# Optimization experiments

Hardware: AMD Instinct MI355X
Metric: run time of the kernel (lower is better)

The kernel has to match this reference:

```python
import jax, jax.numpy as jnp
import numpy as np

NTOKEN, NINP, NHID = 50257, 256, 256
B, T = 64, 2048
RES, FC1 = 10, NHID // 3
EPS = 1e-5

def lrelu(x, p=0.01):
    return jnp.maximum(x, x * p)

def setup_inputs() -> dict:
    key = jax.random.key(0)
    ks = jax.random.split(key, 12)
    s = 0.05
    inp = {
        "input": jax.random.randint(ks[0], (B, T), 0, NTOKEN),
        "hx": jnp.zeros((B, NHID), jnp.float32),
        "cx": jnp.zeros((B, NHID), jnp.float32),
        "seq_len": jax.random.randint(ks[1], (B,), 1, T + 1),  # lengths in [1, T]
        "emb_w": jax.random.uniform(ks[2], (NTOKEN, NINP), jnp.float32, -0.1, 0.1),
        "W_ih": jax.random.normal(ks[3], (4 * NHID, NINP), jnp.float32) * s,
        "W_hh": jax.random.normal(ks[4], (4 * NHID, NHID), jnp.float32) * s,
        "b_ih": jnp.zeros((4 * NHID,), jnp.float32),
        "b_hh": jnp.zeros((4 * NHID,), jnp.float32),
        "rfc1_w": jax.random.normal(ks[5], (RES, NHID), jnp.float32) * s,
        "rfc1_b": jnp.zeros((RES,), jnp.float32),
        "rbn_g": jnp.ones((RES,), jnp.float32),
        "rbn_b": jnp.zeros((RES,), jnp.float32),
        "rbn_rm": jnp.zeros((RES,), jnp.float32),
        "rbn_rv": jnp.ones((RES,), jnp.float32),
        "rfc2_w": jax.random.normal(ks[6], (NHID, RES), jnp.float32) * s,
        "rfc2_b": jnp.zeros((NHID,), jnp.float32),
        "fc1_w": jax.random.normal(ks[7], (FC1, NHID), jnp.float32) * s,
        "fc1_b": jnp.zeros((FC1,), jnp.float32),
        "bn1_g": jnp.ones((FC1,), jnp.float32),
        "bn1_b": jnp.zeros((FC1,), jnp.float32),
        "bn1_rm": jnp.zeros((FC1,), jnp.float32),
        "bn1_rv": jnp.ones((FC1,), jnp.float32),
        "fc2_w": jax.random.normal(ks[8], (2, FC1), jnp.float32) * s,
        "fc2_b": jnp.zeros((2,), jnp.float32),
    }
    return inp

def reference(input, hx, cx, seq_len, emb_w, W_ih, W_hh, b_ih, b_hh,
              rfc1_w, rfc1_b, rbn_g, rbn_b, rbn_rm, rbn_rv, rfc2_w, rfc2_b,
              fc1_w, fc1_b, bn1_g, bn1_b, bn1_rm, bn1_rv, fc2_w, fc2_b):
    # eval mode: dropout = identity, noise = 0, BatchNorm uses running stats
    emb = emb_w[input.T]  # [T, B, ninp]
    # precompute input-side gates once (batched matmul) -> [T, B, 4*nhid]
    x_gates = jnp.einsum('tbi,gi->tbg', emb, W_ih) + b_ih + b_hh

    def step(carry, xg):
        h, c = carry
        gates = xg + h @ W_hh.T
        i, f, g, o = jnp.split(gates, 4, axis=-1)
        c = jax.nn.sigmoid(f) * c + jax.nn.sigmoid(i) * jnp.tanh(g)
        h = jax.nn.sigmoid(o) * jnp.tanh(c)
        return (h, c), h

    (hx_f, cx_f), outs = jax.lax.scan(step, (hx, cx), x_gates)  # outs: [T, B, nhid]

    # ragged mean pooling over first seq_len[b] steps
    mask = (jnp.arange(T)[:, None] < seq_len[None, :]).astype(outs.dtype)  # [T, B]
    feature = jnp.einsum('tbh,tb->bh', outs, mask) / seq_len[:, None].astype(outs.dtype)

    # ResNet block (eval)
    res = jax.nn.relu(feature) @ rfc1_w.T + rfc1_b
    res = jax.nn.relu(res)
    res = (res - rbn_rm) * jax.lax.rsqrt(rbn_rv + EPS) * rbn_g + rbn_b
    feature = feature + res @ rfc2_w.T + rfc2_b

    # classifier head
    fc = feature @ fc1_w.T + fc1_b
    fc = (fc - bn1_rm) * jax.lax.rsqrt(bn1_rv + EPS) * bn1_g + bn1_b
    fc = lrelu(fc)
    logits = fc @ fc2_w.T + fc2_b
    logp = jax.nn.log_softmax(logits, axis=-1)
    return (logp, hx_f, cx_f)
```

## Files before the change

### kernel.cpp

```cpp
#include <hip/hip_runtime.h>
#include <cstdint>


#define NTOKEN 50257
#define NINP 256
#define NHID 256
#define BB 64
#define TT 2048
#define NRES 10
#define NFC1 85
#define EPSV 1e-5f

typedef _Float16 f16;
typedef _Float16 f16x2 __attribute__((ext_vector_type(2)));
typedef _Float16 f16x8 __attribute__((ext_vector_type(8)));
typedef float f32x4 __attribute__((ext_vector_type(4)));

static __device__ __forceinline__ float sigm(float x) { return 1.0f / (1.0f + __expf(-x)); }
static __device__ __forceinline__ float tanh_(float x) {
  float ax = fabsf(x);
  float e = __expf(-2.0f * ax);
  float t = (1.0f - e) / (1.0f + e);
  return x < 0.0f ? -t : t;
}

static __device__ __forceinline__ float fdot2(f16x2 a, f16x2 b, float c) {
#if __has_builtin(__builtin_amdgcn_fdot2)
  return __builtin_amdgcn_fdot2(a, b, c, false);
#else
  return c + (float)a[0] * (float)b[0] + (float)a[1] * (float)b[1];
#endif
}

__global__ void k0_convert(const float* __restrict__ emb_w, const float* __restrict__ W_ih,
                           const float* __restrict__ b_ih, const float* __restrict__ b_hh,
                           f16* __restrict__ emb16, f16* __restrict__ wih16,
                           float* __restrict__ bias) {
  int64_t i = (int64_t)blockIdx.x * blockDim.x + threadIdx.x;
  if (i < (int64_t)NTOKEN * NINP) emb16[i] = (f16)emb_w[i];
  if (i < 4 * NHID * NINP) wih16[i] = (f16)W_ih[i];
  if (i < 4 * NHID) bias[i] = b_ih[i] + b_hh[i];
}

__global__ __launch_bounds__(256) void k1_gemm(const f16* __restrict__ emb16,
                                               const f16* __restrict__ wih16,
                                               const float* __restrict__ bias,
                                               f16* __restrict__ xgtab) {
  __shared__ __align__(16) f16 a_lds[64][40];
  __shared__ __align__(16) f16 b_lds[256][40];
  const int mt = blockIdx.x;
  const int nt0 = blockIdx.y * 256;
  const int tid = threadIdx.x;
  const int lane = tid & 63;
  const int w = tid >> 6;
  const int quad = lane >> 4;
  const int l16 = lane & 15;

  f32x4 acc[16];
#pragma unroll
  for (int i = 0; i < 16; i++) acc[i] = (f32x4){0.f, 0.f, 0.f, 0.f};

  const int ar = tid >> 2;
  int av = mt * 64 + ar;
  if (av > NTOKEN - 1) av = NTOKEN - 1;
  const int ac = (tid & 3) * 8;

  for (int kb = 0; kb < 256; kb += 32) {
    *(uint4*)&a_lds[ar][ac] = *(const uint4*)&emb16[av * 256 + kb + ac];
    {
      const uint4* bs = (const uint4*)&wih16[(nt0 + tid) * 256 + kb];
      uint4* bd = (uint4*)&b_lds[tid][0];
      bd[0] = bs[0]; bd[1] = bs[1]; bd[2] = bs[2]; bd[3] = bs[3];
    }
    __syncthreads();
    f16x8 af = *(const f16x8*)&a_lds[w * 16 + l16][quad * 8];
#pragma unroll
    for (int nt = 0; nt < 16; nt++) {
      f16x8 bf = *(const f16x8*)&b_lds[nt * 16 + l16][quad * 8];
      acc[nt] = __builtin_amdgcn_mfma_f32_16x16x32_f16(af, bf, acc[nt], 0, 0, 0);
    }
    __syncthreads();
  }
#pragma unroll
  for (int nt = 0; nt < 16; nt++) {
#pragma unroll
    for (int rg = 0; rg < 4; rg++) {
      int v = mt * 64 + w * 16 + quad * 4 + rg;
      if (v < NTOKEN) {
        int n = nt0 + nt * 16 + l16;
        xgtab[v * 1024 + n] = (f16)(acc[nt][rg] + bias[n]);
      }
    }
  }
}

#define RK 92
#define LK 36
__global__ __launch_bounds__(512, 2) void k2_rnn(
    const int* __restrict__ input, const float* __restrict__ hx0,
    const float* __restrict__ cx0, const int* __restrict__ seq_len,
    const float* __restrict__ Whh, const f16* __restrict__ xgtab,
    float* __restrict__ feat, float* __restrict__ out_hx, float* __restrict__ out_cx) {
  __shared__ uint2 lw2[LK * 512];
  __shared__ __align__(16) f16 hpak[NHID];
  __shared__ float fo_f[NHID];
  __shared__ float fo_o[NHID];

  const int b = blockIdx.x;
  const int tid = threadIdx.x;
  const int r0 = tid, r1 = tid + 512;

  unsigned int w0[RK], w1[RK];
#pragma unroll
  for (int m = 0; m < 128; m++) {
    float2 a = *(const float2*)&Whh[r0 * 256 + 2 * m];
    float2 d = *(const float2*)&Whh[r1 * 256 + 2 * m];
    f16x2 pa; pa[0] = (f16)a.x; pa[1] = (f16)a.y;
    f16x2 pd; pd[0] = (f16)d.x; pd[1] = (f16)d.y;
    unsigned int ua = __builtin_bit_cast(unsigned int, pa);
    unsigned int ud = __builtin_bit_cast(unsigned int, pd);
    if (m < RK) { w0[m] = ua; w1[m] = ud; }
    else { lw2[(m - RK) * 512 + tid] = make_uint2(ua, ud); }
  }

  float c = 0.0f, pool = 0.0f, hnew = 0.0f;
  if (tid < NHID) {
    hpak[tid] = (f16)hx0[b * NHID + tid];
    c = cx0[b * NHID + tid];
  }
  const int L = seq_len[b];
  __syncthreads();

  const int* tokp = input + b * TT;
  int tok_next = tokp[1];
  f16 xga, xgb;
  {
    int tok0 = tokp[0];
    xga = xgtab[tok0 * 1024 + r0];
    xgb = xgtab[tok0 * 1024 + r1];
  }

  for (int t = 0; t < TT; t++) {
    int tn = (t + 2 < TT) ? tokp[t + 2] : 0;
    f16 pfa = xgtab[tok_next * 1024 + r0];
    f16 pfb = xgtab[tok_next * 1024 + r1];

    float acc0 = (float)xga, acc1 = (float)xgb;
    const uint4* hp = (const uint4*)hpak;
#pragma unroll
    for (int mb = 0; mb < 32; mb++) {
      uint4 h4 = hp[mb];
#pragma unroll
      for (int j = 0; j < 4; j++) {
        const int m = mb * 4 + j;
        unsigned int hu = (j == 0) ? h4.x : (j == 1) ? h4.y : (j == 2) ? h4.z : h4.w;
        f16x2 hh = __builtin_bit_cast(f16x2, hu);
        f16x2 wa, wb;
        if (m < RK) {
          wa = __builtin_bit_cast(f16x2, w0[m]);
          wb = __builtin_bit_cast(f16x2, w1[m]);
        } else {
          uint2 ww = lw2[(m - RK) * 512 + tid];
          wa = __builtin_bit_cast(f16x2, ww.x);
          wb = __builtin_bit_cast(f16x2, ww.y);
        }
        acc0 = fdot2(wa, hh, acc0);
        acc1 = fdot2(wb, hh, acc1);
      }
    }

    if (tid >= NHID) {
      fo_f[tid - NHID] = sigm(acc0);
      fo_o[tid - NHID] = sigm(acc1);
    }
    __syncthreads();
    if (tid < NHID) {
      float ig = sigm(acc0);
      float gg = tanh_(acc1);
      c = fo_f[tid] * c + ig * gg;
      hnew = fo_o[tid] * tanh_(c);
      if (t < L) pool += hnew;
      hpak[tid] = (f16)hnew;
    }
    __syncthreads();
    xga = pfa; xgb = pfb; tok_next = tn;
  }

  if (tid < NHID) {
    feat[b * NHID + tid] = pool / (float)L;
    out_hx[b * NHID + tid] = hnew;
    out_cx[b * NHID + tid] = c;
  }
}

__global__ __launch_bounds__(256) void k3_head(const float* __restrict__ feat,
    const float* __restrict__ rfc1_w, const float* __restrict__ rfc1_b,
    const float* __restrict__ rbn_g, const float* __restrict__ rbn_b,
    const float* __restrict__ rbn_rm, const float* __restrict__ rbn_rv,
    const float* __restrict__ rfc2_w, const float* __restrict__ rfc2_b,
    const float* __restrict__ fc1_w, const float* __restrict__ fc1_b,
    const float* __restrict__ bn1_g, const float* __restrict__ bn1_b,
    const float* __restrict__ bn1_rm, const float* __restrict__ bn1_rv,
    const float* __restrict__ fc2_w, const float* __restrict__ fc2_b,
    float* __restrict__ logp) {
  __shared__ float f[256];
  __shared__ float f2[256];
  __shared__ float res[16];
  __shared__ float fcv[96];
  const int b = blockIdx.x, tid = threadIdx.x;
  const int wv = tid >> 6, lane = tid & 63;
  f[tid] = feat[b * 256 + tid];
  __syncthreads();
  for (int r = wv; r < NRES; r += 4) {
    float p = 0.f;
#pragma unroll
    for (int j0 = 0; j0 < 4; j0++) {
      int j = lane * 4 + j0;
      p += fmaxf(f[j], 0.f) * rfc1_w[r * 256 + j];
    }
    for (int off = 32; off > 0; off >>= 1) p += __shfl_down(p, off);
    if (lane == 0) {
      float x = p + rfc1_b[r];
      x = fmaxf(x, 0.f);
      x = (x - rbn_rm[r]) * rsqrtf(rbn_rv[r] + EPSV) * rbn_g[r] + rbn_b[r];
      res[r] = x;
    }
  }
  __syncthreads();
  {
    float s = rfc2_b[tid];
#pragma unroll
    for (int r = 0; r < NRES; r++) s += res[r] * rfc2_w[tid * NRES + r];
    f2[tid] = f[tid] + s;
  }
  __syncthreads();
  for (int o = wv; o < NFC1; o += 4) {
    float p = 0.f;
#pragma unroll
    for (int j0 = 0; j0 < 4; j0++) {
      int j = lane * 4 + j0;
      p += f2[j] * fc1_w[o * 256 + j];
    }
    for (int off = 32; off > 0; off >>= 1) p += __shfl_down(p, off);
    if (lane == 0) {
      float x = p + fc1_b[o];
      x = (x - bn1_rm[o]) * rsqrtf(bn1_rv[o] + EPSV) * bn1_g[o] + bn1_b[o];
      x = fmaxf(x, 0.01f * x);
      fcv[o] = x;
    }
  }
  __syncthreads();
  if (tid == 0) {
    float l0 = fc2_b[0], l1 = fc2_b[1];
    for (int o2 = 0; o2 < NFC1; o2++) {
      l0 += fcv[o2] * fc2_w[o2];
      l1 += fcv[o2] * fc2_w[NFC1 + o2];
    }
    float mx = fmaxf(l0, l1);
    float lse = mx + __logf(__expf(l0 - mx) + __expf(l1 - mx));
    logp[b * 2 + 0] = l0 - lse;
    logp[b * 2 + 1] = l1 - lse;
  }
}

extern "C" void kernel_launch(void* const* d_in, const int* in_sizes, int n_in,
                              void* d_out, int out_size, void* d_ws, size_t ws_size,
                              hipStream_t stream) {
  const int*   input  = (const int*)  d_in[0];
  const float* hx     = (const float*)d_in[1];
  const float* cx     = (const float*)d_in[2];
  const int*   seqlen = (const int*)  d_in[3];
  const float* emb_w  = (const float*)d_in[4];
  const float* W_ih   = (const float*)d_in[5];
  const float* W_hh   = (const float*)d_in[6];
  const float* b_ih   = (const float*)d_in[7];
  const float* b_hh   = (const float*)d_in[8];
  const float* rfc1_w = (const float*)d_in[9];
  const float* rfc1_b = (const float*)d_in[10];
  const float* rbn_g  = (const float*)d_in[11];
  const float* rbn_b  = (const float*)d_in[12];
  const float* rbn_rm = (const float*)d_in[13];
  const float* rbn_rv = (const float*)d_in[14];
  const float* rfc2_w = (const float*)d_in[15];
  const float* rfc2_b = (const float*)d_in[16];
  const float* fc1_w  = (const float*)d_in[17];
  const float* fc1_b  = (const float*)d_in[18];
  const float* bn1_g  = (const float*)d_in[19];
  const float* bn1_b  = (const float*)d_in[20];
  const float* bn1_rm = (const float*)d_in[21];
  const float* bn1_rv = (const float*)d_in[22];
  const float* fc2_w  = (const float*)d_in[23];
  const float* fc2_b  = (const float*)d_in[24];

  char* ws = (char*)d_ws;
  f16*   emb16 = (f16*)(ws);
  f16*   wih16 = (f16*)(ws + 25731584);
  float* bias  = (float*)(ws + 26255872);
  f16*   xgtab = (f16*)(ws + 26259968);
  float* feat  = (float*)(ws + 129186304);

  float* out = (float*)d_out;

  k0_convert<<<dim3(NTOKEN), 256, 0, stream>>>(emb_w, W_ih, b_ih, b_hh, emb16, wih16, bias);
  k1_gemm<<<dim3((NTOKEN + 63) / 64, 4), 256, 0, stream>>>(emb16, wih16, bias, xgtab);
  k2_rnn<<<dim3(BB), 512, 0, stream>>>(input, hx, cx, seqlen, W_hh, xgtab, feat,
                                       out + 128, out + 128 + BB * NHID);
  k3_head<<<dim3(BB), 256, 0, stream>>>(feat, rfc1_w, rfc1_b, rbn_g, rbn_b, rbn_rm, rbn_rv,
                                        rfc2_w, rfc2_b, fc1_w, fc1_b, bn1_g, bn1_b, bn1_rm,
                                        bn1_rv, fc2_w, fc2_b, out);
}
```

Baseline: 4.165 ms.

## Split LSTM recurrence across 1024 threads with K-partitioned weights and readlane broadcast

Restructures the recurrent kernel so each of 1024 threads owns one hidden unit's four gate rows over a quarter of the K dimension, holding most weights in registers and the rest in LDS. A separate pack kernel pre-converts W_hh to fp16 in this layout. Partial sums are reduced through LDS, and h values are broadcast with readlane instead of LDS vector reads. The aim is shorter per-step dot-product latency and fewer LDS reads on the serial critical path. In exchange it adds a cross-partition reduction and a one-block-per-batch launch at 1024 threads. The pack buffers reuse workspace memory that earlier kernels already consumed.

```diff
diff --git a/kernel.cpp b/kernel.cpp
--- a/kernel.cpp
+++ b/kernel.cpp
@@ -11,6 +11,9 @@
 #define NFC1 85
 #define EPSV 1e-5f
 
+#define QP 23
+#define LJ 9
+
 typedef _Float16 f16;
 typedef _Float16 f16x2 __attribute__((ext_vector_type(2)));
 typedef _Float16 f16x8 __attribute__((ext_vector_type(8)));
@@ -24,11 +27,12 @@
   return x < 0.0f ? -t : t;
 }
 
-static __device__ __forceinline__ float fdot2(f16x2 a, f16x2 b, float c) {
+static __device__ __forceinline__ float fdot2u(unsigned int a, unsigned int b, float c) {
 #if __has_builtin(__builtin_amdgcn_fdot2)
-  return __builtin_amdgcn_fdot2(a, b, c, false);
+  return __builtin_amdgcn_fdot2(__builtin_bit_cast(f16x2, a), __builtin_bit_cast(f16x2, b), c, false);
 #else
-  return c + (float)a[0] * (float)b[0] + (float)a[1] * (float)b[1];
+  f16x2 av = __builtin_bit_cast(f16x2, a), bv = __builtin_bit_cast(f16x2, b);
+  return c + (float)av[0] * (float)bv[0] + (float)av[1] * (float)bv[1];
 #endif
 }
 
@@ -94,102 +98,115 @@
   }
 }
 
-#define RK 92
-#define LK 36
-__global__ __launch_bounds__(512, 2) void k2_rnn(
+__global__ __launch_bounds__(128) void k0b_pack(const float* __restrict__ Whh,
+                                                unsigned int* __restrict__ wregq,
+                                                unsigned int* __restrict__ wldsq) {
+  const int R = blockIdx.x;
+  const int p = threadIdx.x;
+  float2 a = *(const float2*)&Whh[R * 256 + 2 * p];
+  f16x2 pk; pk[0] = (f16)a.x; pk[1] = (f16)a.y;
+  unsigned int uu = __builtin_bit_cast(unsigned int, pk);
+  int u = (R & 255) + 256 * (p >> 5);
+  int ri = R >> 8;
+  int pp = p & 31;
+  if (pp < QP) wregq[(pp * 1024 + u) * 4 + ri] = uu;
+  else         wldsq[((pp - QP) * 1024 + u) * 4 + ri] = uu;
+}
+
+__global__ __launch_bounds__(1024) void k2_rnn(
     const int* __restrict__ input, const float* __restrict__ hx0,
     const float* __restrict__ cx0, const int* __restrict__ seq_len,
-    const float* __restrict__ Whh, const f16* __restrict__ xgtab,
+    const uint4* __restrict__ wregq, const uint4* __restrict__ wldsq,
+    const f16* __restrict__ xgtab,
     float* __restrict__ feat, float* __restrict__ out_hx, float* __restrict__ out_cx) {
-  __shared__ uint2 lw2[LK * 512];
-  __shared__ __align__(16) f16 hpak[NHID];
-  __shared__ float fo_f[NHID];
-  __shared__ float fo_o[NHID];
+  __shared__ uint4 lw4[LJ * 1024];
+  __shared__ float part[3 * 256 * 4];
+  __shared__ f16 xbuf[1024];
+  __shared__ __align__(8) f16 hpak[NHID];
 
   const int b = blockIdx.x;
-  const int tid = threadIdx.x;
-  const int r0 = tid, r1 = tid + 512;
-
-  unsigned int w0[RK], w1[RK];
-#pragma unroll
-  for (int m = 0; m < 128; m++) {
-    float2 a = *(const float2*)&Whh[r0 * 256 + 2 * m];
-    float2 d = *(const float2*)&Whh[r1 * 256 + 2 * m];
-    f16x2 pa; pa[0] = (f16)a.x; pa[1] = (f16)a.y;
-    f16x2 pd; pd[0] = (f16)d.x; pd[1] = (f16)d.y;
-    unsigned int ua = __builtin_bit_cast(unsigned int, pa);
-    unsigned int ud = __builtin_bit_cast(unsigned int, pd);
-    if (m < RK) { w0[m] = ua; w1[m] = ud; }
-    else { lw2[(m - RK) * 512 + tid] = make_uint2(ua, ud); }
-  }
-
-  float c = 0.0f, pool = 0.0f, hnew = 0.0f;
-  if (tid < NHID) {
-    hpak[tid] = (f16)hx0[b * NHID + tid];
-    c = cx0[b * NHID + tid];
+  const int u = threadIdx.x;
+  const int lane = u & 63;
+  const int r = u & 255;
+  const int q = u >> 8;
+
+  uint4 w4[QP];
+#pragma unroll
+  for (int i = 0; i < QP; i++) w4[i] = wregq[i * 1024 + u];
+#pragma unroll
+  for (int j = 0; j < LJ; j++) lw4[j * 1024 + u] = wldsq[j * 1024 + u];
+
+  float c = 0.f, pool = 0.f, h = 0.f;
+  if (u < NHID) {
+    hpak[u] = (f16)hx0[b * NHID + u];
+    c = cx0[b * NHID + u];
   }
   const int L = seq_len[b];
-  __syncthreads();
-
   const int* tokp = input + b * TT;
-  int tok_next = tokp[1];
-  f16 xga, xgb;
   {
-    int tok0 = tokp[0];
-    xga = xgtab[tok0 * 1024 + r0];
-    xgb = xgtab[tok0 * 1024 + r1];
-  }
-
+    int tok0 = __builtin_amdgcn_readfirstlane(tokp[0]);
+    xbuf[u] = xgtab[(size_t)tok0 * 1024 + u];
+  }
+  __syncthreads();
+
+  const unsigned int* hpu = (const unsigned int*)hpak;
+  const int hoff = 32 * q + (lane & 31);
+  unsigned int hsel = hpu[hoff];
+
+  int toff = 0;
+#pragma unroll 1
   for (int t = 0; t < TT; t++) {
-    int tn = (t + 2 < TT) ? tokp[t + 2] : 0;
-    f16 pfa = xgtab[tok_next * 1024 + r0];
-    f16 pfb = xgtab[tok_next * 1024 + r1];
-
-    float acc0 = (float)xga, acc1 = (float)xgb;
-    const uint4* hp = (const uint4*)hpak;
-#pragma unroll
-    for (int mb = 0; mb < 32; mb++) {
-      uint4 h4 = hp[mb];
-#pragma unroll
-      for (int j = 0; j < 4; j++) {
-        const int m = mb * 4 + j;
-        unsigned int hu = (j == 0) ? h4.x : (j == 1) ? h4.y : (j == 2) ? h4.z : h4.w;
-        f16x2 hh = __builtin_bit_cast(f16x2, hu);
-        f16x2 wa, wb;
-        if (m < RK) {
-          wa = __builtin_bit_cast(f16x2, w0[m]);
-          wb = __builtin_bit_cast(f16x2, w1[m]);
-        } else {
-          uint2 ww = lw2[(m - RK) * 512 + tid];
-          wa = __builtin_bit_cast(f16x2, ww.x);
-          wb = __builtin_bit_cast(f16x2, ww.y);
-        }
-        acc0 = fdot2(wa, hh, acc0);
-        acc1 = fdot2(wb, hh, acc1);
-      }
-    }
-
-    if (tid >= NHID) {
-      fo_f[tid - NHID] = sigm(acc0);
-      fo_o[tid - NHID] = sigm(acc1);
+    int tk = __builtin_amdgcn_readfirstlane(tokp[(t + 1 < TT) ? t + 1 : TT - 1]);
+    f16 xn = xgtab[(size_t)tk * 1024 + u];
+
+    float a0 = 0.f, a1 = 0.f, a2 = 0.f, a3 = 0.f;
+#pragma unroll
+    for (int i = 0; i < QP; i++) {
+      unsigned int hs = (unsigned int)__builtin_amdgcn_readlane((int)hsel, i);
+      a0 = fdot2u(w4[i].x, hs, a0);
+      a1 = fdot2u(w4[i].y, hs, a1);
+      a2 = fdot2u(w4[i].z, hs, a2);
+      a3 = fdot2u(w4[i].w, hs, a3);
+    }
+#pragma unroll
+    for (int j = 0; j < LJ; j++) {
+      int je = j + toff; if (je >= LJ) je -= LJ;
+      uint4 w = lw4[je * 1024 + u];
+      unsigned int hs = (unsigned int)__builtin_amdgcn_readlane((int)hsel, QP + je);
+      a0 = fdot2u(w.x, hs, a0);
+      a1 = fdot2u(w.y, hs, a1);
+      a2 = fdot2u(w.z, hs, a2);
+      a3 = fdot2u(w.w, hs, a3);
+    }
+
+    if (q > 0) {
+      *(float4*)&part[((q - 1) * 256 + r) * 4] = make_float4(a0, a1, a2, a3);
     }
     __syncthreads();
-    if (tid < NHID) {
-      float ig = sigm(acc0);
-      float gg = tanh_(acc1);
-      c = fo_f[tid] * c + ig * gg;
-      hnew = fo_o[tid] * tanh_(c);
-      if (t < L) pool += hnew;
-      hpak[tid] = (f16)hnew;
+    if (q == 0) {
+      float4 p1 = *(const float4*)&part[(0 * 256 + r) * 4];
+      float4 p2 = *(const float4*)&part[(1 * 256 + r) * 4];
+      float4 p3 = *(const float4*)&part[(2 * 256 + r) * 4];
+      float gi = a0 + p1.x + p2.x + p3.x + (float)xbuf[r];
+      float gf = a1 + p1.y + p2.y + p3.y + (float)xbuf[NHID + r];
+      float gg = a2 + p1.z + p2.z + p3.z + (float)xbuf[2 * NHID + r];
+      float go = a3 + p1.w + p2.w + p3.w + (float)xbuf[3 * NHID + r];
+      float ig = sigm(gi), fg = sigm(gf), gt = tanh_(gg), og = sigm(go);
+      c = fg * c + ig * gt;
+      h = og * tanh_(c);
+      pool += (t < L) ? h : 0.f;
+      hpak[r] = (f16)h;
     }
     __syncthreads();
-    xga = pfa; xgb = pfb; tok_next = tn;
-  }
-
-  if (tid < NHID) {
-    feat[b * NHID + tid] = pool / (float)L;
-    out_hx[b * NHID + tid] = hnew;
-    out_cx[b * NHID + tid] = c;
+    hsel = hpu[hoff];
+    xbuf[u] = xn;
+    toff++; if (toff == LJ) toff = 0;
+  }
+
+  if (q == 0) {
+    feat[b * NHID + r] = pool / (float)L;
+    out_hx[b * NHID + r] = h;
+    out_cx[b * NHID + r] = c;
   }
 }
 
@@ -299,12 +316,17 @@
   f16*   xgtab = (f16*)(ws + 26259968);
   float* feat  = (float*)(ws + 129186304);
 
+  unsigned int* wregq = (unsigned int*)(ws);
+  unsigned int* wldsq = (unsigned int*)(ws + 376832);
+
   float* out = (float*)d_out;
 
   k0_convert<<<dim3(NTOKEN), 256, 0, stream>>>(emb_w, W_ih, b_ih, b_hh, emb16, wih16, bias);
   k1_gemm<<<dim3((NTOKEN + 63) / 64, 4), 256, 0, stream>>>(emb16, wih16, bias, xgtab);
-  k2_rnn<<<dim3(BB), 512, 0, stream>>>(input, hx, cx, seqlen, W_hh, xgtab, feat,
-                                       out + 128, out + 128 + BB * NHID);
+  k0b_pack<<<dim3(1024), 128, 0, stream>>>(W_hh, wregq, wldsq);
+  k2_rnn<<<dim3(BB), 1024, 0, stream>>>(input, hx, cx, seqlen, (const uint4*)wregq,
+                                        (const uint4*)wldsq, xgtab, feat,
+                                        out + 128, out + 128 + BB * NHID);
   k3_head<<<dim3(BB), 256, 0, stream>>>(feat, rfc1_w, rfc1_b, rbn_g, rbn_b, rbn_rm, rbn_rv,
                                         rfc2_w, rfc2_b, fc1_w, fc1_b, bn1_g, bn1_b, bn1_rm,
                                         bn1_rv, fc2_w, fc2_b, out);
```

Result: slower. 4.355 ms (+4.6%).
